# Optimization experiments

Measured on AMD Instinct MI355X. Metric: run time of the kernel, lower is better.

The kernel has to match this reference:

```python
import jax, jax.numpy as jnp
import numpy as np

N_TOPICS = 1024
TOPIC_DIM = 128
HIDDEN = 512
N_HEADS = 8
HEAD_DIM = HIDDEN // N_HEADS
N_LAYERS = 2
ALPHA = 0.2
TIME_DECAY = 0.1
BATCH = 8


def setup_inputs() -> dict:
    key = jax.random.key(0)
    ks = jax.random.split(key, 16)
    inp = {
        'topic_ids': jax.random.randint(ks[0], (BATCH,), 0, N_TOPICS, dtype=jnp.int32),
        'adj_matrix': jax.random.randint(ks[1], (BATCH, N_TOPICS, N_TOPICS), 0, 2, dtype=jnp.int32),
        'time_matrix': jax.random.uniform(ks[2], (BATCH, N_TOPICS, N_TOPICS), dtype=jnp.float32),
        'attractiveness': jax.random.normal(ks[3], (BATCH,), dtype=jnp.float32),
        # parameters (torch Linear convention: W [out,in], y = x@W.T + b)
        'topic_embedding': jax.random.normal(ks[4], (N_TOPICS, TOPIC_DIM), dtype=jnp.float32) * 0.1,
        'struct_W': jax.random.normal(ks[5], (HIDDEN, TOPIC_DIM), dtype=jnp.float32) * 0.05,
        'struct_b': jnp.zeros((HIDDEN,), dtype=jnp.float32),
        'attract_W': jax.random.normal(ks[6], (HIDDEN, 1), dtype=jnp.float32) * 0.05,
        'attract_b': jnp.zeros((HIDDEN,), dtype=jnp.float32),
        'gat_W': jax.random.normal(ks[7], (N_LAYERS, N_HEADS, HIDDEN, HEAD_DIM), dtype=jnp.float32) * 0.05,
        'gat_a': jax.random.normal(ks[8], (N_LAYERS, N_HEADS, 2 * HEAD_DIM, 1), dtype=jnp.float32) * 0.05,
        'fc1_W': jax.random.normal(ks[9], (HIDDEN, HIDDEN), dtype=jnp.float32) * 0.05,
        'fc1_b': jnp.zeros((HIDDEN,), dtype=jnp.float32),
        'fc2_W': jax.random.normal(ks[10], (1, HIDDEN), dtype=jnp.float32) * 0.05,
        'fc2_b': jnp.zeros((1,), dtype=jnp.float32),
    }
    return inp


def _gat_layer(node, adj, time_w, W, a):
    # node: [B,N,F], adj: [B,N,N] (0/1), time_w: [B,N,N]
    # W: [H,F,hd], a: [H,2*hd,1]
    h = jnp.einsum('bni,hio->bhno', node, W)  # [B,H,N,hd]
    # Additive attention: a = [a_src; a_dst] so e_ij = LeakyReLU(h_i.a_src + h_j.a_dst)
    a_src = a[:, :HEAD_DIM, 0]   # [H,hd]
    a_dst = a[:, HEAD_DIM:, 0]   # [H,hd]
    e_src = jnp.einsum('bhnd,hd->bhn', h, a_src)  # [B,H,N]
    e_dst = jnp.einsum('bhnd,hd->bhn', h, a_dst)  # [B,H,N]
    e = e_src[:, :, :, None] + e_dst[:, :, None, :]  # [B,H,N,N]
    e = jax.nn.leaky_relu(e, negative_slope=ALPHA)
    e = e * time_w[:, None, :, :]
    e = jnp.where(adj[:, None, :, :] == 0, -jnp.inf, e)
    attn = jax.nn.softmax(e, axis=-1)
    out = jnp.einsum('bhij,bhjd->bhid', attn, h)  # [B,H,N,hd]
    out = out.transpose(0, 2, 1, 3).reshape(node.shape[0], node.shape[1], -1)
    return jax.nn.elu(out)


def reference(topic_ids, adj_matrix, time_matrix, attractiveness,
              topic_embedding, struct_W, struct_b, attract_W, attract_b,
              gat_W, gat_a, fc1_W, fc1_b, fc2_W, fc2_b):
    # structural features for all topics -> hidden
    struct = topic_embedding @ struct_W.T + struct_b          # [N,hidden]
    attract = attractiveness[:, None] @ attract_W.T + attract_b  # [B,hidden]
    node = jnp.broadcast_to(struct[None], (BATCH, N_TOPICS, HIDDEN))
    # weighted co-occurrence time (eq.17)
    time_w = jnp.exp(-TIME_DECAY * (time_matrix.max() - time_matrix))  # [B,N,N]
    for l in range(N_LAYERS):
        node = _gat_layer(node, adj_matrix, time_w, gat_W[l], gat_a[l])
    # gather per-sample topic node feature
    topic_feat = jnp.take_along_axis(node, topic_ids[:, None, None].astype(jnp.int32), axis=1)[:, 0]  # [B,hidden]
    combined = topic_feat + attract
    hidden = jax.nn.relu(combined @ fc1_W.T + fc1_b)
    pred = hidden @ fc2_W.T + fc2_b  # [B,1]
    return pred
```

## Files before the change

### kernel.cpp

```cpp
#include <hip/hip_runtime.h>

#define NT 1024
#define TD 128
#define HID 512
#define NH 8
#define HD 64
#define NB 8

typedef unsigned short us;
typedef _Float16 h16;
typedef h16 half8 __attribute__((ext_vector_type(8)));
typedef h16 h16x2 __attribute__((ext_vector_type(2)));
typedef float f32x4 __attribute__((ext_vector_type(4)));

#define LOG2E 1.44269504f

extern "C" __device__ _Float16 __ocml_exp2_f16(_Float16);

__device__ __forceinline__ us f2h(float x) { return __builtin_bit_cast(us, (h16)x); }
__device__ __forceinline__ float h2f(us s) { return (float)__builtin_bit_cast(h16, s); }
__device__ __forceinline__ unsigned int pkh2(float a, float b) {
    auto v = __builtin_amdgcn_cvt_pkrtz(a, b);
    return __builtin_bit_cast(unsigned int, v);
}

__global__ __launch_bounds__(256) void kprep(const float* __restrict__ tm, const int* __restrict__ adj,
                                             float* __restrict__ part, us* __restrict__ TWb,
                                             const float* __restrict__ emb, const float* __restrict__ sW,
                                             const float* __restrict__ sb, us* __restrict__ node0b,
                                             const float* __restrict__ gW, us* __restrict__ Wt,
                                             const float* __restrict__ ga, us* __restrict__ VAVS,
                                             const float* __restrict__ fc2b, float* __restrict__ out) {
    __shared__ __align__(16) float smf[8768];
    int bx = blockIdx.x, t = threadIdx.x;
    if (bx < 1024) {
        const float4* tm4 = (const float4*)tm;
        const int4* ad4 = (const int4*)adj;
        size_t base = (size_t)bx * 256 + t;
        const float C = 0.1f * LOG2E;
        const float NANF = __uint_as_float(0x7FC00000u);
        float m = -1e30f;
        #pragma unroll
        for (int k = 0; k < 8; k++) {
            size_t fi = base + (size_t)k * 262144;
            float4 v = tm4[fi];
            int4 av = ad4[fi];
            m = fmaxf(m, fmaxf(fmaxf(v.x, v.y), fmaxf(v.z, v.w)));
            float w0 = exp2f(v.x * C) * LOG2E;
            float w1 = exp2f(v.y * C) * LOG2E;
            float w2 = exp2f(v.z * C) * LOG2E;
            float w3 = exp2f(v.w * C) * LOG2E;
            w0 = av.x ? w0 : NANF;
            w1 = av.y ? w1 : NANF;
            w2 = av.z ? w2 : NANF;
            w3 = av.w ? w3 : NANF;
            uint2 pk;
            pk.x = pkh2(w0, w1);
            pk.y = pkh2(w2, w3);
            *(uint2*)&TWb[fi * 4] = pk;
        }
        smf[t] = m; __syncthreads();
        for (int s = 128; s > 0; s >>= 1) { if (t < s) smf[t] = fmaxf(smf[t], smf[t + s]); __syncthreads(); }
        if (t == 0) part[bx] = smf[0];
    } else if (bx < 1152) {
        int g = bx - 1024; int iblk = g & 15, oseg = g >> 4;
        us* As = (us*)smf;
        us* Bs = (us*)smf + 64 * 136;
        const float4* esrc = (const float4*)(emb + (size_t)iblk * 64 * TD);
        const float4* wsrc = (const float4*)(sW + (size_t)oseg * 64 * TD);
        #pragma unroll
        for (int rep = 0; rep < 8; rep++) {
            int f = rep * 256 + t;
            int row = f >> 5, c4 = f & 31;
            float4 av = esrc[f];
            float4 bv = wsrc[f];
            uint2 pa, pb;
            pa.x = pkh2(av.x, av.y); pa.y = pkh2(av.z, av.w);
            pb.x = pkh2(bv.x, bv.y); pb.y = pkh2(bv.z, bv.w);
            *(uint2*)&As[row * 136 + c4 * 4] = pa;
            *(uint2*)&Bs[row * 136 + c4 * 4] = pb;
        }
        __syncthreads();
        int l = t & 63, w = t >> 6, m = l & 15, q = l >> 4;
        f32x4 acc[4];
        #pragma unroll
        for (int ot = 0; ot < 4; ot++) acc[ot] = (f32x4){0.f, 0.f, 0.f, 0.f};
        #pragma unroll
        for (int ks = 0; ks < 4; ks++) {
            half8 a = *(const half8*)&As[(w * 16 + m) * 136 + ks * 32 + q * 8];
            #pragma unroll
            for (int ot = 0; ot < 4; ot++) {
                half8 b = *(const half8*)&Bs[(ot * 16 + m) * 136 + ks * 32 + q * 8];
                acc[ot] = __builtin_amdgcn_mfma_f32_16x16x32_f16(a, b, acc[ot], 0, 0, 0);
            }
        }
        #pragma unroll
        for (int ot = 0; ot < 4; ot++) {
            int col = oseg * 64 + ot * 16 + m;
            float sbv = sb[col];
            #pragma unroll
            for (int rr = 0; rr < 4; rr++) {
                int rowi = iblk * 64 + w * 16 + q * 4 + rr;
                node0b[(size_t)rowi * HID + col] = f2h(acc[ot][rr] + sbv);
            }
        }
    } else if (bx < 1280) {
        int g = bx - 1152; int lh = g >> 3, kt = g & 7;
        if (g == 0 && t < NB) out[t] = fc2b[0];
        float* tile = smf;
        const float4* src = (const float4*)(gW + ((size_t)lh * HID + kt * 64) * HD);
        #pragma unroll
        for (int rep = 0; rep < 4; rep++) {
            int f = rep * 256 + t;
            float4 v = src[f];
            int row = f >> 4, col = (f & 15) * 4;
            float* d = tile + row * 65 + col;
            d[0] = v.x; d[1] = v.y; d[2] = v.z; d[3] = v.w;
        }
        __syncthreads();
        int o = t >> 2, ks = (t & 3) * 16;
        us pk[16];
        #pragma unroll
        for (int j = 0; j < 16; j++) pk[j] = f2h(tile[(ks + j) * 65 + o]);
        us* dst = Wt + (size_t)lh * HD * HID + (size_t)o * HID + kt * 64 + ks;
        *(uint4*)dst = *(uint4*)pk;
        *(uint4*)(dst + 8) = *(uint4*)&pk[8];
    } else {
        int g = bx - 1280; int h = g >> 3, iseg = g & 7;
        if (t < 128) {
            int sel = t >> 6, il = t & 63;
            int i = iseg * 64 + il;
            const float* W2row = gW + (size_t)NH * HID * HD + ((size_t)h * HID + i) * HD;
            const float* a2 = ga + NH * 2 * HD + h * 2 * HD;
            const float* av = sel ? a2 : (a2 + HD);
            float s = 0.f;
            #pragma unroll 8
            for (int o = 0; o < HD; o++) s = fmaf(W2row[o], av[o], s);
            VAVS[(size_t)(sel * 8 + h) * HID + i] = f2h(s);
        }
    }
}

__device__ __forceinline__ void gemm_body(const us* __restrict__ A, const us* __restrict__ W,
                                          const float* __restrict__ gav,
                                          us* __restrict__ outT,
                                          float* __restrict__ esO, float* __restrict__ edO,
                                          int iblk, int b, int h, int t, us* sm) {
    us* As = sm;
    us* Bs = sm + 2 * 4608;
    int row = t >> 2, ks = t & 3;
    int l = t & 63, w = t >> 6, m = l & 15, q = l >> 4;
    size_t arow0 = (size_t)(b * NT + iblk * 64);
    const us* ar = A + (arow0 + row) * HID + ks * 16;
    const us* br = W + ((size_t)(h * HD + row)) * HID + ks * 16;
    f32x4 acc[4];
    #pragma unroll
    for (int ot = 0; ot < 4; ot++) acc[ot] = (f32x4){0.f, 0.f, 0.f, 0.f};
    {
        uint4 x0 = *(const uint4*)ar, x1 = *(const uint4*)(ar + 8);
        uint4 y0 = *(const uint4*)br, y1 = *(const uint4*)(br + 8);
        *(uint4*)&As[row * 72 + ks * 16] = x0; *(uint4*)&As[row * 72 + ks * 16 + 8] = x1;
        *(uint4*)&Bs[row * 72 + ks * 16] = y0; *(uint4*)&Bs[row * 72 + ks * 16 + 8] = y1;
    }
    uint4 a0 = *(const uint4*)(ar + 64), a1 = *(const uint4*)(ar + 72);
    uint4 b0 = *(const uint4*)(br + 64), b1 = *(const uint4*)(br + 72);
    for (int it = 0; it < 8; it++) {
        int cur = it & 1, nxt = cur ^ 1;
        uint4 na0, na1, nb0, nb1;
        if (it < 6) {
            int k0 = (it + 2) * 64;
            na0 = *(const uint4*)(ar + k0); na1 = *(const uint4*)(ar + k0 + 8);
            nb0 = *(const uint4*)(br + k0); nb1 = *(const uint4*)(br + k0 + 8);
        }
        __syncthreads();
        if (it < 7) {
            *(uint4*)&As[nxt * 4608 + row * 72 + ks * 16] = a0;
            *(uint4*)&As[nxt * 4608 + row * 72 + ks * 16 + 8] = a1;
            *(uint4*)&Bs[nxt * 4608 + row * 72 + ks * 16] = b0;
            *(uint4*)&Bs[nxt * 4608 + row * 72 + ks * 16 + 8] = b1;
        }
        const us* Ac = As + cur * 4608; const us* Bc = Bs + cur * 4608;
        #pragma unroll
        for (int kt = 0; kt < 2; kt++) {
            half8 av = *(const half8*)&Ac[(w * 16 + m) * 72 + kt * 32 + q * 8];
            #pragma unroll
            for (int ot = 0; ot < 4; ot++) {
                half8 bv = *(const half8*)&Bc[(ot * 16 + m) * 72 + kt * 32 + q * 8];
                acc[ot] = __builtin_amdgcn_mfma_f32_16x16x32_f16(av, bv, acc[ot], 0, 0, 0);
            }
        }
        if (it < 6) { a0 = na0; a1 = na1; b0 = nb0; b1 = nb1; }
    }
    const float* gas = gav + h * 2 * HD;
    float gs[4], gd[4];
    #pragma unroll
    for (int ot = 0; ot < 4; ot++) { gs[ot] = gas[ot * 16 + m]; gd[ot] = gas[HD + ot * 16 + m]; }
    size_t ebase = ((size_t)b * NH + h) * NT + iblk * 64;
    #pragma unroll
    for (int rr = 0; rr < 4; rr++) {
        float s = 0.f, d = 0.f;
        #pragma unroll
        for (int ot = 0; ot < 4; ot++) { float v = acc[ot][rr]; s = fmaf(v, gs[ot], s); d = fmaf(v, gd[ot], d); }
        #pragma unroll
        for (int mask = 1; mask < 16; mask <<= 1) { s += __shfl_xor(s, mask); d += __shfl_xor(d, mask); }
        if (m == 0) {
            int rowi = w * 16 + q * 4 + rr;
            esO[ebase + rowi] = s;
            edO[ebase + rowi] = d;
        }
    }
    #pragma unroll
    for (int ot = 0; ot < 4; ot++) {
        int col = h * HD + ot * 16 + m;
        #pragma unroll
        for (int rr = 0; rr < 4; rr++) {
            int i_loc = w * 16 + q * 4 + rr;
            outT[(size_t)col * NT + iblk * 64 + i_loc] = f2h(acc[ot][rr]);
        }
    }
}

__global__ __launch_bounds__(256) void kgemm1(const us* __restrict__ node0b, const us* __restrict__ Wt,
                                              const float* __restrict__ ga, us* __restrict__ Ht1,
                                              float* __restrict__ es1, float* __restrict__ ed1) {
    __shared__ __align__(16) us sm[4 * 4608];
    int g = blockIdx.x;
    gemm_body(node0b, Wt, ga, Ht1, es1, ed1, g & 15, 0, g >> 4, threadIdx.x, sm);
}

__device__ __forceinline__ unsigned int p_word_fly(unsigned int tw, unsigned int ed, h16x2 es) {
    h16x2 t = __builtin_bit_cast(h16x2, tw);
    h16x2 d = __builtin_bit_cast(h16x2, ed);
    h16x2 e = es + d;
    h16x2 lk = e * (h16)0.2f;
    h16x2 el = __builtin_elementwise_max(e, lk);
    h16x2 mm = t * el;
    h16x2 p;
    p.x = __ocml_exp2_f16(mm.x);
    p.y = __ocml_exp2_f16(mm.y);
    h16x2 z = {(h16)0.0f, (h16)0.0f};
    h16x2 r = __builtin_elementwise_max(p, z);
    return __builtin_bit_cast(unsigned int, r);
}

__device__ __forceinline__ half8 p_frag(uint4 T, uint4 D, h16x2 es) {
    uint4 r;
    r.x = p_word_fly(T.x, D.x, es);
    r.y = p_word_fly(T.y, D.y, es);
    r.z = p_word_fly(T.z, D.z, es);
    r.w = p_word_fly(T.w, D.w, es);
    return __builtin_bit_cast(half8, r);
}

__global__ __launch_bounds__(256) void kattn1(const us* __restrict__ TWb, const us* __restrict__ Ht,
                                              const float* __restrict__ es1, const float* __restrict__ ed1,
                                              const float* __restrict__ part, us* __restrict__ node1b) {
    int n = blockIdx.x;
    int b = n & 7, k = n >> 3;
    int i2 = k & 7, h = k >> 3;
    int t = threadIdx.x;
    __shared__ __align__(16) us Hs[2][64 * 72];
    __shared__ __align__(16) us edl[NT];
    __shared__ float invl_s[128];
    __shared__ float reds[256];
    int l = t & 63, w = t >> 6, m = l & 15, q = l >> 4;
    {
        float pm = fmaxf(fmaxf(part[t * 4], part[t * 4 + 1]), fmaxf(part[t * 4 + 2], part[t * 4 + 3]));
        reds[t] = pm; __syncthreads();
        for (int s = 128; s > 0; s >>= 1) { if (t < s) reds[t] = fmaxf(reds[t], reds[t + s]); __syncthreads(); }
    }
    float sfac = exp2f(-reds[0] * (0.1f * LOG2E));
    {
        float4 ev = *(const float4*)&ed1[h * NT + t * 4];
        uint2 pk; pk.x = pkh2(ev.x * sfac, ev.y * sfac); pk.y = pkh2(ev.z * sfac, ev.w * sfac);
        *(uint2*)&edl[t * 4] = pk;
    }
    int rowA = i2 * 128 + w * 32 + m;
    h16 eA = (h16)(es1[h * NT + rowA] * sfac);
    h16 eB = (h16)(es1[h * NT + rowA + 16] * sfac);
    h16x2 esvA = {eA, eA}, esvB = {eB, eB};
    const us* twA = TWb + ((size_t)(b * NT) + rowA) * NT + q * 8;
    const us* twB = twA + (size_t)16 * NT;
    int hr = t >> 2, js = t & 3;
    const us* htrow = Ht + ((size_t)(h * HD) + hr) * NT + js * 16;
    f32x4 acc[2][4];
    #pragma unroll
    for (int ti = 0; ti < 2; ti++)
        #pragma unroll
        for (int ot = 0; ot < 4; ot++) acc[ti][ot] = (f32x4){0.f, 0.f, 0.f, 0.f};
    f32x4 acc1[2] = {(f32x4){0.f, 0.f, 0.f, 0.f}, (f32x4){0.f, 0.f, 0.f, 0.f}};
    h16 ov = (m == 0) ? (h16)1.0f : (h16)0.0f;
    half8 bones = {ov, ov, ov, ov, ov, ov, ov, ov};
    uint4 H0 = *(const uint4*)htrow, H1 = *(const uint4*)(htrow + 8);
    *(uint4*)&Hs[0][hr * 72 + js * 16] = H0;
    *(uint4*)&Hs[0][hr * 72 + js * 16 + 8] = H1;
    H0 = *(const uint4*)(htrow + 64); H1 = *(const uint4*)(htrow + 72);
    uint4 TA0 = *(const uint4*)twA,        TA1 = *(const uint4*)(twA + 32);
    uint4 TB0 = *(const uint4*)twB,        TB1 = *(const uint4*)(twB + 32);
    __syncthreads();
    for (int it = 0; it < 16; it++) {
        int cur = it & 1, nxt = cur ^ 1;
        int j0 = it * 64;
        uint4 nH0, nH1, nA0, nA1, nB0, nB1;
        if (it < 14) {
            nH0 = *(const uint4*)(htrow + j0 + 128);
            nH1 = *(const uint4*)(htrow + j0 + 136);
        }
        if (it < 15) {
            nA0 = *(const uint4*)(twA + j0 + 64);  nA1 = *(const uint4*)(twA + j0 + 96);
            nB0 = *(const uint4*)(twB + j0 + 64);  nB1 = *(const uint4*)(twB + j0 + 96);
        }
        uint4 D0 = *(const uint4*)&edl[j0 + q * 8];
        uint4 D1 = *(const uint4*)&edl[j0 + 32 + q * 8];
        half8 pA0 = p_frag(TA0, D0, esvA);
        half8 pA1 = p_frag(TA1, D1, esvA);
        half8 pB0 = p_frag(TB0, D0, esvB);
        half8 pB1 = p_frag(TB1, D1, esvB);
        __syncthreads();
        if (it < 15) {
            *(uint4*)&Hs[nxt][hr * 72 + js * 16] = H0;
            *(uint4*)&Hs[nxt][hr * 72 + js * 16 + 8] = H1;
        }
        const us* Hc = Hs[cur];
        #pragma unroll
        for (int ot = 0; ot < 4; ot++) {
            half8 bv0 = *(const half8*)&Hc[(ot * 16 + m) * 72 + q * 8];
            half8 bv1 = *(const half8*)&Hc[(ot * 16 + m) * 72 + 32 + q * 8];
            acc[0][ot] = __builtin_amdgcn_mfma_f32_16x16x32_f16(pA0, bv0, acc[0][ot], 0, 0, 0);
            acc[0][ot] = __builtin_amdgcn_mfma_f32_16x16x32_f16(pA1, bv1, acc[0][ot], 0, 0, 0);
            acc[1][ot] = __builtin_amdgcn_mfma_f32_16x16x32_f16(pB0, bv0, acc[1][ot], 0, 0, 0);
            acc[1][ot] = __builtin_amdgcn_mfma_f32_16x16x32_f16(pB1, bv1, acc[1][ot], 0, 0, 0);
        }
        acc1[0] = __builtin_amdgcn_mfma_f32_16x16x32_f16(pA0, bones, acc1[0], 0, 0, 0);
        acc1[0] = __builtin_amdgcn_mfma_f32_16x16x32_f16(pA1, bones, acc1[0], 0, 0, 0);
        acc1[1] = __builtin_amdgcn_mfma_f32_16x16x32_f16(pB0, bones, acc1[1], 0, 0, 0);
        acc1[1] = __builtin_amdgcn_mfma_f32_16x16x32_f16(pB1, bones, acc1[1], 0, 0, 0);
        if (it < 14) { H0 = nH0; H1 = nH1; }
        if (it < 15) { TA0 = nA0; TA1 = nA1; TB0 = nB0; TB1 = nB1; }
    }
    if (m == 0) {
        #pragma unroll
        for (int rr = 0; rr < 4; rr++) {
            invl_s[w * 32 + q * 4 + rr]      = 1.f / acc1[0][rr];
            invl_s[w * 32 + 16 + q * 4 + rr] = 1.f / acc1[1][rr];
        }
    }
    __syncthreads();
    size_t rbase = (size_t)(b * NT + i2 * 128);
    #pragma unroll
    for (int ti = 0; ti < 2; ti++) {
        #pragma unroll
        for (int ot = 0; ot < 4; ot++) {
            int col = h * HD + ot * 16 + m;
            #pragma unroll
            for (int rr = 0; rr < 4; rr++) {
                int rloc = w * 32 + ti * 16 + q * 4 + rr;
                float v = acc[ti][ot][rr] * invl_s[rloc];
                v = v > 0.f ? v : (__expf(v) - 1.f);
                node1b[(rbase + rloc) * HID + col] = f2h(v);
            }
        }
    }
}

__global__ __launch_bounds__(256) void kctx(const us* __restrict__ TWb, const us* __restrict__ node1b,
                                            const us* __restrict__ VAVS, const float* __restrict__ part,
                                            const int* __restrict__ topic_ids,
                                            float* __restrict__ ctxp, float* __restrict__ pl) {
    int n = blockIdx.x;
    int b = n & 7, jb = n >> 3;
    int t = threadIdx.x;
    __shared__ __align__(16) us n1s[32 * 520];
    __shared__ __align__(16) us vvs[16 * 520];
    __shared__ __align__(16) us qrow[HID];
    __shared__ float Ps[8][33];
    __shared__ float es2q[8];
    __shared__ float reds[256];
    int qi = topic_ids[b];
    {
        float pm = fmaxf(fmaxf(part[t * 4], part[t * 4 + 1]), fmaxf(part[t * 4 + 2], part[t * 4 + 3]));
        reds[t] = pm; __syncthreads();
        for (int s = 128; s > 0; s >>= 1) { if (t < s) reds[t] = fmaxf(reds[t], reds[t + s]); __syncthreads(); }
    }
    float sfac = exp2f(-reds[0] * (0.1f * LOG2E));
    {
        int row = t >> 3, c = (t & 7) * 64;
        const uint4* src = (const uint4*)(node1b + ((size_t)(b * NT) + jb * 32 + row) * HID + c);
        uint4* dst = (uint4*)&n1s[row * 520 + c];
        #pragma unroll
        for (int k = 0; k < 8; k++) dst[k] = src[k];
    }
    {
        int row = t >> 4, c = (t & 15) * 32;
        const uint4* src = (const uint4*)(VAVS + (size_t)row * HID + c);
        uint4* dst = (uint4*)&vvs[row * 520 + c];
        dst[0] = src[0]; dst[1] = src[1]; dst[2] = src[2]; dst[3] = src[3];
    }
    if (t < 32) {
        const uint4* src = (const uint4*)(node1b + ((size_t)(b * NT) + qi) * HID + t * 16);
        *(uint4*)&qrow[t * 16] = src[0];
        *(uint4*)&qrow[t * 16 + 8] = src[1];
    }
    __syncthreads();
    {
        int h = t >> 5, li = t & 31;
        float s = 0.f;
        #pragma unroll 4
        for (int ii = 0; ii < 16; ii++) {
            int i = li * 16 + ii;
            s = fmaf(h2f(qrow[i]), h2f(vvs[(8 + h) * 520 + i]), s);
        }
        #pragma unroll
        for (int mask = 1; mask < 32; mask <<= 1) s += __shfl_xor(s, mask);
        if (li == 0) es2q[h] = s;
    }
    __syncthreads();
    int l = t & 63, w = t >> 6, m = l & 15, q = l >> 4;
    if (w < 2) {
        f32x4 acc = (f32x4){0.f, 0.f, 0.f, 0.f};
        #pragma unroll
        for (int kt = 0; kt < 16; kt++) {
            half8 a = *(const half8*)&n1s[(w * 16 + m) * 520 + kt * 32 + q * 8];
            half8 bv = *(const half8*)&vvs[m * 520 + kt * 32 + q * 8];
            acc = __builtin_amdgcn_mfma_f32_16x16x32_f16(a, bv, acc, 0, 0, 0);
        }
        if (m < 8) {
            const us* twq = TWb + ((size_t)(b * NT) + qi) * NT + jb * 32;
            float esv = es2q[m];
            #pragma unroll
            for (int r = 0; r < 4; r++) {
                int j = w * 16 + q * 4 + r;
                float e = esv + acc[r];
                e = fmaxf(e, 0.2f * e);
                float twu = h2f(twq[j]);
                float p = fmaxf(exp2f(twu * sfac * e), 0.f);
                Ps[m][j] = p;
            }
        }
    }
    __syncthreads();
    {
        int h = t >> 5, j = t & 31;
        float s = Ps[h][j];
        #pragma unroll
        for (int mask = 1; mask < 32; mask <<= 1) s += __shfl_xor(s, mask);
        if (j == 0) pl[((size_t)b * NH + h) * 32 + jb] = s;
    }
    float ac[8][2];
    #pragma unroll
    for (int h = 0; h < 8; h++) { ac[h][0] = 0.f; ac[h][1] = 0.f; }
    for (int j = 0; j < 32; j++) {
        unsigned int uv = *(const unsigned int*)&n1s[j * 520 + t * 2];
        h16x2 hv = __builtin_bit_cast(h16x2, uv);
        float f0 = (float)hv.x, f1 = (float)hv.y;
        #pragma unroll
        for (int h = 0; h < 8; h++) {
            float p = Ps[h][j];
            ac[h][0] = fmaf(p, f0, ac[h][0]);
            ac[h][1] = fmaf(p, f1, ac[h][1]);
        }
    }
    float* cp = ctxp + (((size_t)b * 32 + jb) * NH) * HID;
    #pragma unroll
    for (int h = 0; h < 8; h++) {
        float2 v; v.x = ac[h][0]; v.y = ac[h][1];
        *(float2*)&cp[h * HID + t * 2] = v;
    }
}

__global__ __launch_bounds__(256) void kcomb(const float* __restrict__ ctxp, const float* __restrict__ pl,
                                             const us* __restrict__ Wt2, const float* __restrict__ attr,
                                             const float* __restrict__ aW, const float* __restrict__ ab,
                                             float* __restrict__ comb) {
    int h = blockIdx.x & 7, b = blockIdx.x >> 3;
    int t = threadIdx.x;
    __shared__ float cx[HID];
    __shared__ float ln[1];
    if (t < 32) {
        float s = pl[((size_t)b * NH + h) * 32 + t];
        #pragma unroll
        for (int mask = 1; mask < 32; mask <<= 1) s += __shfl_xor(s, mask);
        if (t == 0) ln[0] = 1.f / s;
    }
    float a0 = 0.f, a1 = 0.f;
    for (int jb = 0; jb < 32; jb++) {
        const float* cp = ctxp + (((size_t)b * 32 + jb) * NH + h) * HID;
        a0 += cp[t]; a1 += cp[t + 256];
    }
    __syncthreads();
    float li = ln[0];
    cx[t] = a0 * li; cx[t + 256] = a1 * li;
    __syncthreads();
    int o2 = t >> 2, ks = t & 3;
    const us* wrow = Wt2 + ((size_t)h * HD + o2) * HID + ks * 128;
    float s = 0.f;
    #pragma unroll 8
    for (int k = 0; k < 128; k++) s = fmaf(cx[ks * 128 + k], h2f(wrow[k]), s);
    s += __shfl_xor(s, 1); s += __shfl_xor(s, 2);
    if (ks == 0) {
        float v = s > 0.f ? s : (__expf(s) - 1.f);
        int col = h * HD + o2;
        comb[b * HID + col] = v + attr[b] * aW[col] + ab[col];
    }
}

__global__ __launch_bounds__(256) void kfc(const float* __restrict__ comb,
                                           const float* __restrict__ fc1W, const float* __restrict__ fc1b,
                                           const float* __restrict__ fc2W, float* __restrict__ out) {
    int kseg = blockIdx.x, b = blockIdx.y;
    int t = threadIdx.x;
    __shared__ float cs[HID];
    __shared__ float r2[256];
    cs[t] = comb[b * HID + t];
    cs[t + 256] = comb[b * HID + t + 256];
    __syncthreads();
    int kk = kseg * 16 + (t >> 4);
    int j = t & 15;
    const float* row = fc1W + (size_t)kk * HID;
    float acc = 0.f;
    #pragma unroll 8
    for (int mi = 0; mi < 32; mi++) {
        int idx = mi * 16 + j;
        acc = fmaf(cs[idx], row[idx], acc);
    }
    #pragma unroll
    for (int mask = 1; mask < 16; mask <<= 1) acc += __shfl_xor(acc, mask);
    float partv = 0.f;
    if (j == 0) {
        float hk = fmaxf(acc + fc1b[kk], 0.f);
        partv = hk * fc2W[kk];
    }
    r2[t] = partv; __syncthreads();
    for (int s = 128; s > 0; s >>= 1) { if (t < s) r2[t] += r2[t + s]; __syncthreads(); }
    if (t == 0) atomicAdd(&out[b], r2[0]);
}

extern "C" void kernel_launch(void* const* d_in, const int* in_sizes, int n_in,
                              void* d_out, int out_size, void* d_ws, size_t ws_size,
                              hipStream_t stream) {
    const int*   topic_ids = (const int*)d_in[0];
    const int*   adj       = (const int*)d_in[1];
    const float* tm        = (const float*)d_in[2];
    const float* attr      = (const float*)d_in[3];
    const float* emb       = (const float*)d_in[4];
    const float* sW        = (const float*)d_in[5];
    const float* sb        = (const float*)d_in[6];
    const float* aW        = (const float*)d_in[7];
    const float* ab        = (const float*)d_in[8];
    const float* gW        = (const float*)d_in[9];
    const float* ga        = (const float*)d_in[10];
    const float* fc1W      = (const float*)d_in[11];
    const float* fc1b      = (const float*)d_in[12];
    const float* fc2W      = (const float*)d_in[13];
    const float* fc2b      = (const float*)d_in[14];
    float* out = (float*)d_out;

    char* p = (char*)d_ws;
    us* TWb    = (us*)p; p += sizeof(us) * (size_t)NB * NT * NT;
    us* node0b = (us*)p; p += sizeof(us) * (size_t)NT * HID;
    us* Wt     = (us*)p; p += sizeof(us) * (size_t)2 * NH * HD * HID;
    us* Ht1    = (us*)p; p += sizeof(us) * (size_t)HID * NT;
    us* node1b = (us*)p; p += sizeof(us) * (size_t)NB * NT * HID;
    us* VAVS   = (us*)p; p += sizeof(us) * (size_t)16 * HID;
    float* es1  = (float*)p; p += sizeof(float) * NH * NT;
    float* ed1  = (float*)p; p += sizeof(float) * NH * NT;
    float* ctxp = (float*)p; p += sizeof(float) * (size_t)NB * 32 * NH * HID;
    float* pl   = (float*)p; p += sizeof(float) * NB * NH * 32;
    float* comb = (float*)p; p += sizeof(float) * NB * HID;
    float* part = (float*)p; p += sizeof(float) * 1024;

    kprep<<<1344, 256, 0, stream>>>(tm, adj, part, TWb, emb, sW, sb, node0b, gW, Wt, ga, VAVS, fc2b, out);
    kgemm1<<<128, 256, 0, stream>>>(node0b, Wt, ga, Ht1, es1, ed1);
    kattn1<<<512, 256, 0, stream>>>(TWb, Ht1, es1, ed1, part, node1b);
    kctx<<<256, 256, 0, stream>>>(TWb, node1b, VAVS, part, topic_ids, ctxp, pl);
    kcomb<<<64, 256, 0, stream>>>(ctxp, pl, Wt + (size_t)NH * HD * HID, attr, aW, ab, comb);
    kfc<<<dim3(32, NB), 256, 0, stream>>>(comb, fc1W, fc1b, fc2W, out);
}
```

Baseline: 175.9 us.

## Fuse combine and FC tail into one kernel, reduce ctx partials via atomics

kctx now accumulates its per-block context partials straight into a small ctx buffer with float atomics, which kprep zeroes, instead of writing 32 partial slabs per sample. The separate kcomb and kfc kernels are merged into one 8-block kout kernel that normalises, projects, applies ELU plus the attractiveness term, and runs fc1/fc2 directly, writing the output without atomics. This removes one kernel launch and the large partial-context buffer. In exchange it adds atomic contention in kctx and leaves the tail running on only 8 blocks, each doing a serial 512x512 matvec.

```diff
diff --git a/kernel.cpp b/kernel.cpp
--- a/kernel.cpp
+++ b/kernel.cpp
@@ -30,7 +30,7 @@
                                              const float* __restrict__ sb, us* __restrict__ node0b,
                                              const float* __restrict__ gW, us* __restrict__ Wt,
                                              const float* __restrict__ ga, us* __restrict__ VAVS,
-                                             const float* __restrict__ fc2b, float* __restrict__ out) {
+                                             float* __restrict__ ctxz) {
     __shared__ __align__(16) float smf[8768];
     int bx = blockIdx.x, t = threadIdx.x;
     if (bx < 1024) {
@@ -106,7 +106,6 @@
         }
     } else if (bx < 1280) {
         int g = bx - 1152; int lh = g >> 3, kt = g & 7;
-        if (g == 0 && t < NB) out[t] = fc2b[0];
         float* tile = smf;
         const float4* src = (const float4*)(gW + ((size_t)lh * HID + kt * 64) * HD);
         #pragma unroll
@@ -137,6 +136,9 @@
             #pragma unroll 8
             for (int o = 0; o < HD; o++) s = fmaf(W2row[o], av[o], s);
             VAVS[(size_t)(sel * 8 + h) * HID + i] = f2h(s);
+        } else {
+            int zi = (g * 128 + (t - 128)) * 4;
+            *(float4*)&ctxz[zi] = make_float4(0.f, 0.f, 0.f, 0.f);
         }
     }
 }
@@ -366,7 +368,7 @@
 __global__ __launch_bounds__(256) void kctx(const us* __restrict__ TWb, const us* __restrict__ node1b,
                                             const us* __restrict__ VAVS, const float* __restrict__ part,
                                             const int* __restrict__ topic_ids,
-                                            float* __restrict__ ctxp, float* __restrict__ pl) {
+                                            float* __restrict__ ctx, float* __restrict__ pl) {
     int n = blockIdx.x;
     int b = n & 7, jb = n >> 3;
     int t = threadIdx.x;
@@ -460,79 +462,74 @@
             ac[h][1] = fmaf(p, f1, ac[h][1]);
         }
     }
-    float* cp = ctxp + (((size_t)b * 32 + jb) * NH) * HID;
+    float* cp = ctx + ((size_t)b * NH) * HID;
     #pragma unroll
     for (int h = 0; h < 8; h++) {
-        float2 v; v.x = ac[h][0]; v.y = ac[h][1];
-        *(float2*)&cp[h * HID + t * 2] = v;
-    }
-}
-
-__global__ __launch_bounds__(256) void kcomb(const float* __restrict__ ctxp, const float* __restrict__ pl,
-                                             const us* __restrict__ Wt2, const float* __restrict__ attr,
-                                             const float* __restrict__ aW, const float* __restrict__ ab,
-                                             float* __restrict__ comb) {
-    int h = blockIdx.x & 7, b = blockIdx.x >> 3;
+        atomicAdd(&cp[h * HID + t * 2], ac[h][0]);
+        atomicAdd(&cp[h * HID + t * 2 + 1], ac[h][1]);
+    }
+}
+
+__global__ __launch_bounds__(256) void kout(const float* __restrict__ ctx, const float* __restrict__ pl,
+                                            const us* __restrict__ Wt2, const float* __restrict__ attr,
+                                            const float* __restrict__ aW, const float* __restrict__ ab,
+                                            const float* __restrict__ fc1W, const float* __restrict__ fc1b,
+                                            const float* __restrict__ fc2W, const float* __restrict__ fc2b,
+                                            float* __restrict__ out) {
+    int b = blockIdx.x;
     int t = threadIdx.x;
-    __shared__ float cx[HID];
-    __shared__ float ln[1];
-    if (t < 32) {
-        float s = pl[((size_t)b * NH + h) * 32 + t];
+    __shared__ float cxs[NH * HID];
+    __shared__ float comb[HID];
+    __shared__ float linv[NH];
+    __shared__ float r2[256];
+    {
+        int h = t >> 5, j = t & 31;
+        float s = pl[((size_t)b * NH + h) * 32 + j];
         #pragma unroll
         for (int mask = 1; mask < 32; mask <<= 1) s += __shfl_xor(s, mask);
-        if (t == 0) ln[0] = 1.f / s;
-    }
-    float a0 = 0.f, a1 = 0.f;
-    for (int jb = 0; jb < 32; jb++) {
-        const float* cp = ctxp + (((size_t)b * 32 + jb) * NH + h) * HID;
-        a0 += cp[t]; a1 += cp[t + 256];
-    }
-    __syncthreads();
-    float li = ln[0];
-    cx[t] = a0 * li; cx[t + 256] = a1 * li;
-    __syncthreads();
-    int o2 = t >> 2, ks = t & 3;
-    const us* wrow = Wt2 + ((size_t)h * HD + o2) * HID + ks * 128;
-    float s = 0.f;
-    #pragma unroll 8
-    for (int k = 0; k < 128; k++) s = fmaf(cx[ks * 128 + k], h2f(wrow[k]), s);
-    s += __shfl_xor(s, 1); s += __shfl_xor(s, 2);
-    if (ks == 0) {
+        if (j == 0) linv[h] = 1.f / s;
+    }
+    __syncthreads();
+    #pragma unroll
+    for (int rep = 0; rep < 16; rep++) {
+        int i = rep * 256 + t;
+        cxs[i] = ctx[(size_t)b * NH * HID + i] * linv[i >> 9];
+    }
+    __syncthreads();
+    #pragma unroll
+    for (int cc = 0; cc < 2; cc++) {
+        int col = cc * 256 + t;
+        int h = col >> 6;
+        const us* wrow = Wt2 + (size_t)col * HID;
+        const float* cx = &cxs[h * HID];
+        float s = 0.f;
+        #pragma unroll 8
+        for (int k = 0; k < HID; k++) s = fmaf(cx[k], h2f(wrow[k]), s);
         float v = s > 0.f ? s : (__expf(s) - 1.f);
-        int col = h * HD + o2;
-        comb[b * HID + col] = v + attr[b] * aW[col] + ab[col];
-    }
-}
-
-__global__ __launch_bounds__(256) void kfc(const float* __restrict__ comb,
-                                           const float* __restrict__ fc1W, const float* __restrict__ fc1b,
-                                           const float* __restrict__ fc2W, float* __restrict__ out) {
-    int kseg = blockIdx.x, b = blockIdx.y;
-    int t = threadIdx.x;
-    __shared__ float cs[HID];
-    __shared__ float r2[256];
-    cs[t] = comb[b * HID + t];
-    cs[t + 256] = comb[b * HID + t + 256];
-    __syncthreads();
-    int kk = kseg * 16 + (t >> 4);
+        comb[col] = v + attr[b] * aW[col] + ab[col];
+    }
+    __syncthreads();
+    float partv = 0.f;
     int j = t & 15;
-    const float* row = fc1W + (size_t)kk * HID;
-    float acc = 0.f;
-    #pragma unroll 8
-    for (int mi = 0; mi < 32; mi++) {
-        int idx = mi * 16 + j;
-        acc = fmaf(cs[idx], row[idx], acc);
-    }
-    #pragma unroll
-    for (int mask = 1; mask < 16; mask <<= 1) acc += __shfl_xor(acc, mask);
-    float partv = 0.f;
-    if (j == 0) {
-        float hk = fmaxf(acc + fc1b[kk], 0.f);
-        partv = hk * fc2W[kk];
+    for (int g = 0; g < 32; g++) {
+        int kk = g * 16 + (t >> 4);
+        const float* row = fc1W + (size_t)kk * HID;
+        float acc = 0.f;
+        #pragma unroll 8
+        for (int mi = 0; mi < 32; mi++) {
+            int idx = mi * 16 + j;
+            acc = fmaf(comb[idx], row[idx], acc);
+        }
+        #pragma unroll
+        for (int mask = 1; mask < 16; mask <<= 1) acc += __shfl_xor(acc, mask);
+        if (j == 0) {
+            float hk = fmaxf(acc + fc1b[kk], 0.f);
+            partv = fmaf(hk, fc2W[kk], partv);
+        }
     }
     r2[t] = partv; __syncthreads();
     for (int s = 128; s > 0; s >>= 1) { if (t < s) r2[t] += r2[t + s]; __syncthreads(); }
-    if (t == 0) atomicAdd(&out[b], r2[0]);
+    if (t == 0) out[b] = r2[0] + fc2b[0];
 }
 
 extern "C" void kernel_launch(void* const* d_in, const int* in_sizes, int n_in,
@@ -564,15 +561,14 @@
     us* VAVS   = (us*)p; p += sizeof(us) * (size_t)16 * HID;
     float* es1  = (float*)p; p += sizeof(float) * NH * NT;
     float* ed1  = (float*)p; p += sizeof(float) * NH * NT;
-    float* ctxp = (float*)p; p += sizeof(float) * (size_t)NB * 32 * NH * HID;
+    float* ctx  = (float*)p; p += sizeof(float) * (size_t)NB * NH * HID;
     float* pl   = (float*)p; p += sizeof(float) * NB * NH * 32;
-    float* comb = (float*)p; p += sizeof(float) * NB * HID;
     float* part = (float*)p; p += sizeof(float) * 1024;
 
-    kprep<<<1344, 256, 0, stream>>>(tm, adj, part, TWb, emb, sW, sb, node0b, gW, Wt, ga, VAVS, fc2b, out);
+    kprep<<<1344, 256, 0, stream>>>(tm, adj, part, TWb, emb, sW, sb, node0b, gW, Wt, ga, VAVS, ctx);
     kgemm1<<<128, 256, 0, stream>>>(node0b, Wt, ga, Ht1, es1, ed1);
     kattn1<<<512, 256, 0, stream>>>(TWb, Ht1, es1, ed1, part, node1b);
-    kctx<<<256, 256, 0, stream>>>(TWb, node1b, VAVS, part, topic_ids, ctxp, pl);
-    kcomb<<<64, 256, 0, stream>>>(ctxp, pl, Wt + (size_t)NH * HD * HID, attr, aW, ab, comb);
-    kfc<<<dim3(32, NB), 256, 0, stream>>>(comb, fc1W, fc1b, fc2W, out);
-}
+    kctx<<<256, 256, 0, stream>>>(TWb, node1b, VAVS, part, topic_ids, ctx, pl);
+    kout<<<8, 256, 0, stream>>>(ctx, pl, Wt + (size_t)NH * HD * HID, attr, aW, ab,
+                                fc1W, fc1b, fc2W, fc2b, out);
+}
```

Result: slower. 249.8 us (+42.0%).
